# Performance work log

Measured on AMD Instinct MI355X. Metric: run time of the kernel, lower is better.

Reference implementation:

```python
import jax, jax.numpy as jnp
import numpy as np

N = 512           # nodes
DIM = 64          # feature dim (in_dim == dim)
KS = (0.9, 0.7, 0.6)
M_DIM = 17
EDGE_DIM = 1
EIN = 2 * DIM + 1 + EDGE_DIM  # EGNN edge-mlp input width = 130
L = 3             # shared EGNN layers per scale


def _rn(k, shape, s=0.05):
    return jax.random.normal(k, shape, jnp.float32) * s


def setup_inputs() -> dict:
    key = jax.random.key(0)
    k = jax.random.split(key, 12)
    feat = jax.random.normal(k[0], (1, N, DIM), jnp.float32)
    coor = jax.random.normal(k[1], (1, N, 3), jnp.float32)
    # sparse-ish binary adjacency stored densely, as the module expects
    edge = (jax.random.uniform(k[2], (1, N, N, 1)) < 0.05).astype(jnp.float32)
    return {
        "feat": feat, "coor": coor, "edge": edge,
        "We1": _rn(k[3], (L, EIN, 2 * EIN)), "be1": jnp.zeros((L, 2 * EIN), jnp.float32),
        "We2": _rn(k[4], (L, 2 * EIN, M_DIM)), "be2": jnp.zeros((L, M_DIM), jnp.float32),
        "Wc1": _rn(k[5], (L, M_DIM, 4 * M_DIM)), "bc1": jnp.zeros((L, 4 * M_DIM), jnp.float32),
        "Wc2": _rn(k[6], (L, 4 * M_DIM, 1)), "bc2": jnp.zeros((L, 1), jnp.float32),
        "Wn1": _rn(k[7], (L, DIM + M_DIM, 2 * DIM)), "bn1": jnp.zeros((L, 2 * DIM), jnp.float32),
        "Wn2": _rn(k[8], (L, 2 * DIM, DIM)), "bn2": jnp.zeros((L, DIM), jnp.float32),
        "wp": _rn(k[9], (len(KS), DIM)), "bp": jnp.zeros((len(KS),), jnp.float32),
        "ep": 0,
    }


def _egnn(feats, coors, edges, We1, be1, We2, be2, Wc1, bc1, Wc2, bc2,
          Wn1, bn1, Wn2, bn2):
    # feats [B,n,d], coors [B,n,3], edges [B,n,n,1]
    rel = coors[:, :, None, :] - coors[:, None, :, :]           # [B,n,n,3]
    dist = jnp.sum(rel * rel, axis=-1, keepdims=True)           # [B,n,n,1]
    B, n, d = feats.shape
    fi = jnp.broadcast_to(feats[:, :, None, :], (B, n, n, d))
    fj = jnp.broadcast_to(feats[:, None, :, :], (B, n, n, d))
    e_in = jnp.concatenate([fi, fj, dist, edges], axis=-1)      # [B,n,n,EIN]
    m = jax.nn.silu(jax.nn.silu(e_in @ We1 + be1) @ We2 + be2)  # [B,n,n,M]
    cw = jax.nn.silu(m @ Wc1 + bc1) @ Wc2 + bc2                 # [B,n,n,1]
    coors_out = coors + jnp.sum(cw * rel, axis=2)               # [B,n,3]
    m_i = jnp.sum(m, axis=2)                                    # [B,n,M]
    h = jax.nn.silu(jnp.concatenate([feats, m_i], axis=-1) @ Wn1 + bn1) @ Wn2 + bn2
    return feats + h, coors_out


def _forward(feat, coor, edge, We1, be1, We2, be2, Wc1, bc1, Wc2, bc2,
             Wn1, bn1, Wn2, bn2, wp, bp):
    org_h, org_g, org_c = feat[0], edge[0, :, :, 0], coor[0]
    n_nodes = org_h.shape[0]
    ug = (org_g != 0).astype(jnp.float32)
    ug2 = ((ug @ ug) != 0).astype(jnp.float32)  # 2-hop closure adjacency
    hs = []
    for i, kf in enumerate(KS):
        kcnt = max(2, int(kf * n_nodes))
        scores = jax.nn.sigmoid(org_h @ wp[i] + bp[i])          # [n]
        vals, idx = jax.lax.top_k(scores, kcnt)
        h = org_h[idx] * vals[:, None]                          # gather + scale
        g = ug2[idx][:, idx]                                    # row+col gather
        c = org_c[idx]
        hc, coors, edges = h[None], c[None], g[None, :, :, None]
        for j in range(3):
            ht, coors = _egnn(hc, coors, edges,
                              We1[j], be1[j], We2[j], be2[j],
                              Wc1[j], bc1[j], Wc2[j], bc2[j],
                              Wn1[j], bn1[j], Wn2[j], bn2[j])
            hc = jax.nn.relu(hc + ht)
        # unpool: zero-scatter back to original node set
        h_full = jnp.zeros((n_nodes, hc.shape[-1]), hc.dtype).at[idx].set(hc[0])
        hs.append(h_full)
    out = hs[-1]
    for h_i in hs:
        out = jnp.maximum(out, h_i)
    return out


def reference(feat, coor, edge, We1, be1, We2, be2, Wc1, bc1, Wc2, bc2,
              Wn1, bn1, Wn2, bn2, wp, bp, ep):
    return _forward(feat, coor, edge, We1, be1, We2, be2, Wc1, bc1, Wc2, bc2,
                    Wn1, bn1, Wn2, bn2, wp, bp)
```

## Files before the change

kernel.cpp:

```cpp
#include <hip/hip_runtime.h>
#include <hip/hip_bf16.h>

typedef unsigned long long u64;
typedef unsigned int u32;
typedef unsigned short u16;

#define NN   512
#define DIMF 64
#define E2   260
#define KPAD 272
#define MD   17
#define MH   68
#define NH1  128
#define K0   460
#define K1   358
#define K2   307
#define KT   1125
#define O1   460
#define O2   818
#define PADU 1152
#define AS   272
#define NT0  8
#define NT1  6
#define NT2  5
#define T0T   (K0*NT0)
#define T01T  (T0T + K1*NT1)
#define TTOT  (T01T + K2*NT2)
#define PBLK  ((TTOT+3)/4)
#define MSTR  32
#define WVLDS 4096

typedef __attribute__((ext_vector_type(8)))  short short8;
typedef __attribute__((ext_vector_type(16))) float f32x16;

union SF  { int4 i4; u16 us[8]; u32 w[4]; short8 v; };
union F4U { float4 v; float f[4]; };

__device__ __forceinline__ float fast_exp2(float x){
#if __has_builtin(__builtin_amdgcn_exp2f)
    return __builtin_amdgcn_exp2f(x);
#else
    return __expf(x * 0.6931471805599453f);
#endif
}
__device__ __forceinline__ float fast_rcp(float x){
#if __has_builtin(__builtin_amdgcn_rcpf)
    return __builtin_amdgcn_rcpf(x);
#else
    return __fdividef(1.0f, x);
#endif
}
__device__ __forceinline__ float siluf(float x){
    return x * fast_rcp(1.0f + fast_exp2(x * -1.4426950408889634f));
}
__device__ __forceinline__ float sigf(float x){
    return fast_rcp(1.0f + fast_exp2(x * -1.4426950408889634f));
}
__device__ __forceinline__ u16 bf16_rne(float f){
    u32 u = __float_as_uint(f);
    u += 0x7FFFu + ((u >> 16) & 1u);
    return (u16)(u >> 16);
}
__device__ __forceinline__ float bf16f(u16 h){
    return __uint_as_float(((u32)h) << 16);
}
__device__ __forceinline__ u32 pk_bf16(float x, float y){
    float2 f2; f2.x = x; f2.y = y;
    __hip_bfloat162 h = __float22bfloat162_rn(f2);
    union { __hip_bfloat162 b; u32 u; } cv; cv.b = h;
    return cv.u;
}
__device__ __forceinline__ void lgkm_wait(){
#if __has_builtin(__builtin_amdgcn_s_waitcnt)
    __builtin_amdgcn_s_waitcnt(0xC07F);
#endif
}

__global__ __launch_bounds__(256) void k_pre(
    const float* __restrict__ edge, const float* __restrict__ feat,
    const float* __restrict__ wp, const float* __restrict__ bp,
    const float* __restrict__ We2, const float* __restrict__ Wc1,
    const float* __restrict__ We1, const float* __restrict__ be2,
    const float* __restrict__ bc1, const float* __restrict__ Wc2,
    u64* __restrict__ ugw, float* __restrict__ scores,
    u16* __restrict__ W2f, u16* __restrict__ Wc1f,
    float* __restrict__ wdP, float* __restrict__ weP, float* __restrict__ be2P,
    float* __restrict__ bc1P, float* __restrict__ Wc2P, u64* __restrict__ ug2w){
    int blk = blockIdx.x, t = threadIdx.x;
    if (blk < 128){
        int i = blk*4 + (t>>6); int lane = t&63;
        const float* row = edge + (size_t)i*NN;
        for (int w = 0; w < 8; w++){
            u64 m = __ballot(row[w*64+lane] != 0.0f);
            if (lane == 0) ugw[i*8+w] = m;
        }
        return;
    }
    if (blk < 134){
        int gid = (blk-128)*256 + t; if (gid >= 3*NN) return;
        int l = gid>>9, n = gid&511;
        float s = bp[l];
        for (int d = 0; d < DIMF; d++) s = fmaf(feat[n*DIMF+d], wp[l*DIMF+d], s);
        scores[gid] = sigf(s);
        return;
    }
    int idx = (blk-134)*256 + t;
    if (idx < 52224){
        int e = idx&7, lane = (idx>>3)&63, hl = (idx>>9)&1, c = (idx>>10)%17, jl = idx/17408;
        int q = lane>>5, nn = lane&31;
        int k = c*16 + q*8 + e;
        float v = (k < E2 && nn < MD) ? We2[jl*E2*MD + k*MD + nn] : 0.0f;
        u16 hi = bf16_rne(v);
        W2f[idx] = hl ? bf16_rne(v - bf16f(hi)) : hi;
        return;
    }
    idx -= 52224;
    if (idx < 9216){
        int e = idx & 7, lane = (idx>>3)&63, c2 = (idx>>9)&1, T = (idx>>10)%3, jl = idx/3072;
        int q = lane>>5, nn = lane&31;
        int o = c2*16 + q*8 + e, h = T*32 + nn;
        float v = (o < MD && h < MH) ? Wc1[jl*MD*MH + o*MH + h] : 0.0f;
        Wc1f[idx] = bf16_rne(v);
        return;
    }
    idx -= 9216;
    if (idx < 816){ int jl = idx/KPAD, k = idx%KPAD;
        wdP[idx] = (k < E2) ? We1[jl*130*E2 + 128*E2 + k] : 0.0f; return; }
    idx -= 816;
    if (idx < 816){ int jl = idx/KPAD, k = idx%KPAD;
        weP[idx] = (k < E2) ? We1[jl*130*E2 + 129*E2 + k] : 0.0f; return; }
    idx -= 816;
    if (idx < 96){ int jl = idx/32, o = idx%32;
        be2P[idx] = (o < MD) ? be2[jl*MD+o] : 0.0f; return; }
    idx -= 96;
    if (idx < 288){ int jl = idx/96, h = idx%96;
        bc1P[idx] = (h < MH) ? bc1[jl*MH+h] : 0.0f; return; }
    idx -= 288;
    if (idx < 288){ int jl = idx/96, h = idx%96;
        Wc2P[idx] = (h < MH) ? Wc2[jl*MH+h] : 0.0f; return; }
    idx -= 288;
    if (idx < 4096){ ug2w[idx] = 0ULL; return; }
}

__global__ __launch_bounds__(512) void k_sortug2(
    const float* __restrict__ scores, const u64* __restrict__ ugw,
    float* __restrict__ svals, int* __restrict__ sidx, int* __restrict__ rev,
    u64* __restrict__ ug2w){
    int blk = blockIdx.x, t = threadIdx.x;
    if (blk < 3){
        int l = blk;
        __shared__ float sk[NN];
        __shared__ int   si[NN];
        sk[t] = scores[l*NN+t]; si[t] = t; rev[l*NN+t] = -1;
        __syncthreads();
        for (int k = 2; k <= NN; k <<= 1){
            for (int jj = k>>1; jj > 0; jj >>= 1){
                int p = t ^ jj;
                if (p > t){
                    float ka = sk[t], kb = sk[p];
                    int ia = si[t], ib = si[p];
                    bool before = (ka > kb) || (ka == kb && ia < ib);
                    bool sw = ((t & k) == 0) ? (!before) : before;
                    if (sw){ sk[t]=kb; sk[p]=ka; si[t]=ib; si[p]=ia; }
                }
                __syncthreads();
            }
        }
        svals[l*NN+t] = sk[t]; sidx[l*NN+t] = si[t];
        int kcnt = (l==0)?K0:(l==1)?K1:K2;
        if (t < kcnt) rev[l*NN + si[t]] = t;
    } else {
        int gid = (blk-3)*512 + t;
        int i  = gid >> 6;
        int w  = (gid >> 3) & 7;
        int kc = gid & 7;
        u64 rm = ugw[i*8 + kc];
        u64 acc = 0;
        int base = kc*64;
        while (rm){
            int k2 = __builtin_ctzll(rm);
            rm &= rm - 1;
            acc |= ugw[(base + k2)*8 + w];
        }
        if (acc) atomicOr(&ug2w[i*8 + w], acc);
    }
}

__device__ __forceinline__ void ab_comp(int jl, const float* __restrict__ We1,
                                        const float* __restrict__ be1, float hval,
                                        int u, int lane,
                                        float* __restrict__ Ap, float* __restrict__ BF){
    const float* W = We1 + jl*130*E2;
    int r  = 4*lane;
    int rt = 256 + lane;
    int rtc = (lane < 4) ? rt : 256;
    F4U av; av.v = *(const float4*)(be1 + jl*E2 + r);
    F4U bv; bv.f[0]=bv.f[1]=bv.f[2]=bv.f[3]=0.0f;
    float avx = be1[jl*E2 + rtc];
    float bvx = 0.0f;
    for (int d = 0; d < DIMF; d++){
        float hv = __shfl(hval, d);
        F4U w1; w1.v = *(const float4*)(W + d*E2 + r);
        F4U w2; w2.v = *(const float4*)(W + (DIMF+d)*E2 + r);
#pragma unroll
        for (int i = 0; i < 4; i++){
            av.f[i] = fmaf(hv, w1.f[i], av.f[i]);
            bv.f[i] = fmaf(hv, w2.f[i], bv.f[i]);
        }
        avx = fmaf(hv, W[d*E2 + rtc], avx);
        bvx = fmaf(hv, W[(DIMF+d)*E2 + rtc], bvx);
    }
    *(float4*)(Ap + u*AS + r) = av.v;
    *(float4*)(BF + ((size_t)(lane>>1)*PADU + u)*8 + (lane&1)*4) = bv.v;
    if (lane < 16){
        int k = 256 + lane;
        float aval = (lane < 4) ? avx : 0.0f;
        float bval = (lane < 4) ? bvx : 0.0f;
        Ap[u*AS + k] = aval;
        BF[((size_t)(k>>3)*PADU + u)*8 + (k&7)] = bval;
    }
}

__global__ __launch_bounds__(256) void k_gab(
    const float* __restrict__ feat, const float* __restrict__ coor,
    const float* __restrict__ svals, const int* __restrict__ sidx,
    const float* __restrict__ We1, const float* __restrict__ be1,
    float* __restrict__ hc, float* __restrict__ c0, float* __restrict__ c1,
    float* __restrict__ mi, float* __restrict__ Ap, float* __restrict__ BF){
    int t = threadIdx.x; int u = blockIdx.x*4 + (t>>6); if (u >= KT) return;
    int lane = t&63;
    int l = (u<K0)?0:(u<O2)?1:2;
    int a = u - ((l==0)?0:(l==1)?O1:O2);
    int org = sidx[l*NN+a];
    float val = svals[l*NN+a];
    float hval = feat[org*DIMF+lane]*val;
    hc[u*DIMF+lane] = hval;
    if (lane < 3){ float c = coor[org*3+lane]; c0[u*4+lane]=c; c1[u*4+lane]=c; }
    if (lane == 3){ c0[u*4+3]=0.0f; c1[u*4+3]=0.0f; }
    if (lane < 20) mi[u*20+lane] = 0.0f;
    ab_comp(0, We1, be1, hval, u, lane, Ap, BF);
}

template<int DOCW>
__global__ __launch_bounds__(256, 3) void k_pair(
    int jl,
    const float* __restrict__ Ap, const float* __restrict__ BF,
    const u16* __restrict__ W2f, const u16* __restrict__ Wc1f,
    const float* __restrict__ wdP, const float* __restrict__ weP,
    const float* __restrict__ be2P, const float* __restrict__ bc1P,
    const float* __restrict__ Wc2P, const float* __restrict__ bc2,
    const float* __restrict__ cin, float* __restrict__ cout,
    float* __restrict__ mi, const int* __restrict__ sidx,
    const u64* __restrict__ ug2w){
    __shared__ __align__(16) char sWK[4*WVLDS];
    __shared__ __align__(16) char sWD[1088];
    __shared__ __align__(16) char sWE[1088];
    int t = threadIdx.x;
    if (t < 68)       ((float4*)sWD)[t]    = *(const float4*)(wdP + jl*KPAD + 4*t);
    else if (t < 136) ((float4*)sWE)[t-68] = *(const float4*)(weP + jl*KPAD + 4*(t-68));
    int wid0 = blockIdx.x*4 + (t>>6);
    int lane = t&63, n = lane&31, q = lane>>5;
    bool dead = (wid0 >= TTOT);
    int wid = dead ? (TTOT-1) : wid0;
    int l, kl, off, a, tile;
    if (wid < T0T)       { l=0; kl=K0; off=0;  a = wid>>3; tile = wid&7; }
    else if (wid < T01T) { int w = wid-T0T;  l=1; kl=K1; off=O1; a = w/NT1; tile = w - a*NT1; }
    else                 { int w = wid-T01T; l=2; kl=K2; off=O2; a = w/NT2; tile = w - a*NT2; }
    int u = off + a;
    int b0 = tile*64 + n, b1 = b0 + 32;
    float act0 = (b0 < kl) ? 1.0f : 0.0f;
    float act1 = (b1 < kl) ? 1.0f : 0.0f;
    int b0c = min(b0, kl-1), b1c = min(b1, kl-1);
    int ub0 = off + b0c, ub1 = off + b1c;
    int ia  = sidx[l*NN+a];
    int ib0 = sidx[l*NN+b0c], ib1 = sidx[l*NN+b1c];
    float ef0 = act0 * (float)((ug2w[ia*8 + (ib0>>6)] >> (ib0&63)) & 1ULL);
    float ef1 = act1 * (float)((ug2w[ia*8 + (ib1>>6)] >> (ib1&63)) & 1ULL);
    F4U ca;  ca.v  = ((const float4*)cin)[u];
    F4U cb0; cb0.v = ((const float4*)cin)[ub0];
    F4U cb1; cb1.v = ((const float4*)cin)[ub1];
    float tx0 = ca.f[0]-cb0.f[0], ty0 = ca.f[1]-cb0.f[1], tz0 = ca.f[2]-cb0.f[2];
    float tx1 = ca.f[0]-cb1.f[0], ty1 = ca.f[1]-cb1.f[1], tz1 = ca.f[2]-cb1.f[2];
    float dd0 = tx0*tx0 + ty0*ty0 + tz0*tz0;
    float dd1 = tx1*tx1 + ty1*ty1 + tz1*tz1;

    char* myk = sWK + (t>>6)*WVLDS;
    {
        const float* Au = Ap + u*AS;
        ((float4*)myk)[lane] = *(const float4*)(Au + 4*lane);
        if (lane < 4) ((float4*)myk)[64+lane] = *(const float4*)(Au + 256 + 4*lane);
    }
    __syncthreads();

    const float* pB0 = BF + ((size_t)q*PADU + ub0)*8;
    const float* pB1 = BF + ((size_t)q*PADU + ub1)*8;
    const u16*   pW  = W2f + jl*17408 + lane*8;
    const char*  pA  = myk + q*32;
    const char*  pWD = sWD + q*32;
    const char*  pWE = sWE + q*32;

    f32x16 acc0, acc1;
#pragma unroll
    for (int r = 0; r < 16; r++){ acc0[r] = 0.0f; acc1[r] = 0.0f; }

    F4U nb0a, nb0b, nb1a, nb1b; SF nwh, nwl;
    nb0a.v = *(const float4*)(pB0);     nb0b.v = *(const float4*)(pB0 + 4);
    nb1a.v = *(const float4*)(pB1);     nb1b.v = *(const float4*)(pB1 + 4);
    nwh.i4 = *(const int4*)(pW);        nwl.i4 = *(const int4*)(pW + 512);

    for (int c = 0; c < 17; c++){
        F4U b0a = nb0a, b0b = nb0b, b1a = nb1a, b1b = nb1b;
        SF  wh  = nwh,  wl  = nwl;
        pB0 += 2*PADU*8; pB1 += 2*PADU*8; pW += 1024;
        if (c < 16){
            nb0a.v = *(const float4*)(pB0);     nb0b.v = *(const float4*)(pB0 + 4);
            nb1a.v = *(const float4*)(pB1);     nb1b.v = *(const float4*)(pB1 + 4);
            nwh.i4 = *(const int4*)(pW);        nwl.i4 = *(const int4*)(pW + 512);
        }
        F4U a0, a1, w0, w1, e0, e1;
        a0.v = *(const float4*)(pA);       a1.v = *(const float4*)(pA + 16);
        w0.v = *(const float4*)(pWD);      w1.v = *(const float4*)(pWD + 16);
        e0.v = *(const float4*)(pWE);      e1.v = *(const float4*)(pWE + 16);
        pA += 64; pWD += 64; pWE += 64;
        float s0[8], s1[8];
#pragma unroll
        for (int e = 0; e < 4; e++){
            s0[e]   = siluf(fmaf(dd0, w0.f[e], fmaf(ef0, e0.f[e], a0.f[e] + b0a.f[e])));
            s1[e]   = siluf(fmaf(dd1, w0.f[e], fmaf(ef1, e0.f[e], a0.f[e] + b1a.f[e])));
            s0[4+e] = siluf(fmaf(dd0, w1.f[e], fmaf(ef0, e1.f[e], a1.f[e] + b0b.f[e])));
            s1[4+e] = siluf(fmaf(dd1, w1.f[e], fmaf(ef1, e1.f[e], a1.f[e] + b1b.f[e])));
        }
        SF shi0, slo0, shi1, slo1;
#pragma unroll
        for (int p = 0; p < 4; p++){
            float x = s0[2*p], y = s0[2*p+1];
            u32 h = pk_bf16(x, y);
            shi0.w[p] = h;
            slo0.w[p] = pk_bf16(x - __uint_as_float(h << 16),
                                y - __uint_as_float(h & 0xFFFF0000u));
            x = s1[2*p]; y = s1[2*p+1];
            h = pk_bf16(x, y);
            shi1.w[p] = h;
            slo1.w[p] = pk_bf16(x - __uint_as_float(h << 16),
                                y - __uint_as_float(h & 0xFFFF0000u));
        }
        acc0 = __builtin_amdgcn_mfma_f32_32x32x16_bf16(shi0.v, wh.v, acc0, 0, 0, 0);
        acc0 = __builtin_amdgcn_mfma_f32_32x32x16_bf16(slo0.v, wh.v, acc0, 0, 0, 0);
        acc0 = __builtin_amdgcn_mfma_f32_32x32x16_bf16(shi0.v, wl.v, acc0, 0, 0, 0);
        acc1 = __builtin_amdgcn_mfma_f32_32x32x16_bf16(shi1.v, wh.v, acc1, 0, 0, 0);
        acc1 = __builtin_amdgcn_mfma_f32_32x32x16_bf16(slo1.v, wh.v, acc1, 0, 0, 0);
        acc1 = __builtin_amdgcn_mfma_f32_32x32x16_bf16(shi1.v, wl.v, acc1, 0, 0, 0);
    }

    float be2v = be2P[jl*32 + n];
    u16* mlds = (u16*)myk;
    float msum = 0.0f;
#pragma unroll
    for (int r = 0; r < 16; r++){
        int row = (r&3) + 8*(r>>2) + 4*q;
        float m0 = siluf(acc0[r] + be2v);
        float m1 = siluf(acc1[r] + be2v);
        m0 = (tile*64 + row      < kl) ? m0 : 0.0f;
        m1 = (tile*64 + 32 + row < kl) ? m1 : 0.0f;
        msum += m0 + m1;
        if (DOCW){
            mlds[row*MSTR + n]        = bf16_rne(m0);
            mlds[(row+32)*MSTR + n]   = bf16_rne(m1);
        }
    }
    msum += __shfl_xor(msum, 32);
    if (!dead && lane < MD) atomicAdd(&mi[u*20 + lane], msum);

    if (DOCW){
        lgkm_wait();
        const char* mb = (const char*)mlds;
        float gx = 0.0f, gy = 0.0f, gz = 0.0f;
        float bc2v = bc2[jl];
#pragma unroll
        for (int S = 0; S < 2; S++){
            SF af0, af1;
            af0.i4 = *(const int4*)(mb + (S*32+n)*(MSTR*2) + q*16);
            af1.i4 = *(const int4*)(mb + (S*32+n)*(MSTR*2) + 32 + q*16);
            float cwp[16];
#pragma unroll
            for (int r = 0; r < 16; r++) cwp[r] = 0.0f;
            for (int T = 0; T < 3; T++){
                SF bb0, bb1;
                bb0.i4 = *(const int4*)(Wc1f + jl*3072 + T*1024 +       lane*8);
                bb1.i4 = *(const int4*)(Wc1f + jl*3072 + T*1024 + 512 + lane*8);
                f32x16 p2;
#pragma unroll
                for (int r = 0; r < 16; r++) p2[r] = 0.0f;
                p2 = __builtin_amdgcn_mfma_f32_32x32x16_bf16(af0.v, bb0.v, p2, 0, 0, 0);
                p2 = __builtin_amdgcn_mfma_f32_32x32x16_bf16(af1.v, bb1.v, p2, 0, 0, 0);
                float bc1v = bc1P[jl*96 + T*32 + n];
                float wc2v = Wc2P[jl*96 + T*32 + n];
#pragma unroll
                for (int r = 0; r < 16; r++)
                    cwp[r] = fmaf(siluf(p2[r] + bc1v), wc2v, cwp[r]);
            }
#pragma unroll
            for (int r = 0; r < 16; r++){
                int row  = (r&3) + 8*(r>>2) + 4*q + S*32;
                int brow = tile*64 + row;
                F4U cbr; cbr.v = ((const float4*)cin)[off + min(brow, kl-1)];
                float cw = cwp[r] + ((n == 0) ? bc2v : 0.0f);
                cw = (brow < kl) ? cw : 0.0f;
                gx = fmaf(cw, ca.f[0]-cbr.f[0], gx);
                gy = fmaf(cw, ca.f[1]-cbr.f[1], gy);
                gz = fmaf(cw, ca.f[2]-cbr.f[2], gz);
            }
        }
#pragma unroll
        for (int s = 1; s < 64; s <<= 1){
            gx += __shfl_xor(gx, s); gy += __shfl_xor(gy, s); gz += __shfl_xor(gz, s);
        }
        if (!dead && lane == 0){
            atomicAdd(&cout[u*4+0], gx);
            atomicAdd(&cout[u*4+1], gy);
            atomicAdd(&cout[u*4+2], gz);
        }
    }
}

__global__ __launch_bounds__(256) void k_nodeab(
    int jl, int donext, int docopy,
    const float* __restrict__ Wn1, const float* __restrict__ bn1,
    const float* __restrict__ Wn2, const float* __restrict__ bn2,
    const float* __restrict__ We1, const float* __restrict__ be1,
    float* __restrict__ hc, float* __restrict__ mi,
    const float* __restrict__ ccur, float* __restrict__ cnext,
    float* __restrict__ Ap, float* __restrict__ BF){
    int t = threadIdx.x; int u = blockIdx.x*4 + (t>>6); if (u >= KT) return;
    int lane = t&63;
    float hval = hc[u*DIMF+lane];
    float mval = (lane < MD) ? mi[u*20+lane] : 0.0f;
    const float* W1 = Wn1 + jl*(DIMF+MD)*NH1;
    float v0 = bn1[jl*NH1+lane], v1 = bn1[jl*NH1+lane+64];
    for (int d = 0; d < DIMF; d++){
        float x = __shfl(hval, d);
        v0 = fmaf(x, W1[d*NH1+lane],    v0);
        v1 = fmaf(x, W1[d*NH1+lane+64], v1);
    }
    for (int d = 0; d < MD; d++){
        float x = __shfl(mval, d);
        v0 = fmaf(x, W1[(DIMF+d)*NH1+lane],    v0);
        v1 = fmaf(x, W1[(DIMF+d)*NH1+lane+64], v1);
    }
    float s0 = siluf(v0), s1 = siluf(v1);
    const float* W2 = Wn2 + jl*NH1*DIMF;
    float h = bn2[jl*DIMF+lane];
    for (int i = 0; i < 64; i++) h = fmaf(__shfl(s0, i), W2[i*DIMF+lane], h);
    for (int i = 0; i < 64; i++) h = fmaf(__shfl(s1, i), W2[(64+i)*DIMF+lane], h);
    float hn = fmaxf(0.0f, fmaf(2.0f, hval, h));
    hc[u*DIMF+lane] = hn;
    if (donext){
        if (lane < 20) mi[u*20+lane] = 0.0f;
        if (docopy && lane < 4) cnext[u*4+lane] = ccur[u*4+lane];
        ab_comp(jl+1, We1, be1, hn, u, lane, Ap, BF);
    }
}

__global__ void k_final(const float* __restrict__ hc, const int* __restrict__ rev,
                        float* __restrict__ out){
    int gid = blockIdx.x*blockDim.x + threadIdx.x;
    if (gid >= NN*DIMF) return;
    int nn = gid>>6, d = gid&63;
    float v = 0.0f;
    int a0 = rev[0*NN+nn]; if (a0 >= 0) v = fmaxf(v, hc[(0  + a0)*DIMF + d]);
    int a1 = rev[1*NN+nn]; if (a1 >= 0) v = fmaxf(v, hc[(O1 + a1)*DIMF + d]);
    int a2 = rev[2*NN+nn]; if (a2 >= 0) v = fmaxf(v, hc[(O2 + a2)*DIMF + d]);
    out[gid] = v;
}

extern "C" void kernel_launch(void* const* d_in, const int* in_sizes, int n_in,
                              void* d_out, int out_size, void* d_ws, size_t ws_size,
                              hipStream_t stream) {
    (void)in_sizes; (void)n_in; (void)out_size; (void)ws_size;
    const float* feat = (const float*)d_in[0];
    const float* coor = (const float*)d_in[1];
    const float* edge = (const float*)d_in[2];
    const float* We1  = (const float*)d_in[3];
    const float* be1  = (const float*)d_in[4];
    const float* We2  = (const float*)d_in[5];
    const float* be2  = (const float*)d_in[6];
    const float* Wc1  = (const float*)d_in[7];
    const float* bc1  = (const float*)d_in[8];
    const float* Wc2  = (const float*)d_in[9];
    const float* bc2  = (const float*)d_in[10];
    const float* Wn1  = (const float*)d_in[11];
    const float* bn1  = (const float*)d_in[12];
    const float* Wn2  = (const float*)d_in[13];
    const float* bn2  = (const float*)d_in[14];
    const float* wp   = (const float*)d_in[15];
    const float* bp   = (const float*)d_in[16];
    float* out = (float*)d_out;

    char* wsb = (char*)d_ws;
    u64*   ugw    = (u64*)  (wsb + 0);
    u64*   ug2w   = (u64*)  (wsb + 32768);
    float* scores = (float*)(wsb + 65536);
    float* svals  = (float*)(wsb + 71680);
    int*   sidx   = (int*)  (wsb + 77824);
    int*   rev    = (int*)  (wsb + 83968);
    float* c0     = (float*)(wsb + 90112);
    float* c1     = (float*)(wsb + 108544);
    float* mi     = (float*)(wsb + 126976);
    float* hc     = (float*)(wsb + 217088);
    float* Ap     = (float*)(wsb + 505344);
    float* BF     = (float*)(wsb + 1729536);
    u16*   W2f    = (u16*)  (wsb + 2982912);
    u16*   Wc1f   = (u16*)  (wsb + 3087360);
    float* wdP    = (float*)(wsb + 3105792);
    float* weP    = (float*)(wsb + 3109120);
    float* be2P   = (float*)(wsb + 3112448);
    float* bc1P   = (float*)(wsb + 3112832);
    float* Wc2P   = (float*)(wsb + 3113984);

    k_pre<<<399, 256, 0, stream>>>(edge, feat, wp, bp, We2, Wc1, We1, be2, bc1, Wc2,
                                   ugw, scores, W2f, Wc1f,
                                   wdP, weP, be2P, bc1P, Wc2P, ug2w);
    k_sortug2<<<67, 512, 0, stream>>>(scores, ugw, svals, sidx, rev, ug2w);
    k_gab<<<282, 256, 0, stream>>>(feat, coor, svals, sidx, We1, be1,
                                   hc, c0, c1, mi, Ap, BF);
    k_pair<1><<<PBLK, 256, 0, stream>>>(0, Ap, BF, W2f, Wc1f,
                                        wdP, weP, be2P, bc1P, Wc2P, bc2,
                                        c0, c1, mi, sidx, ug2w);
    k_nodeab<<<282, 256, 0, stream>>>(0, 1, 1, Wn1, bn1, Wn2, bn2, We1, be1,
                                      hc, mi, c1, c0, Ap, BF);
    k_pair<1><<<PBLK, 256, 0, stream>>>(1, Ap, BF, W2f, Wc1f,
                                        wdP, weP, be2P, bc1P, Wc2P, bc2,
                                        c1, c0, mi, sidx, ug2w);
    k_nodeab<<<282, 256, 0, stream>>>(1, 1, 0, Wn1, bn1, Wn2, bn2, We1, be1,
                                      hc, mi, c0, c1, Ap, BF);
    k_pair<0><<<PBLK, 256, 0, stream>>>(2, Ap, BF, W2f, Wc1f,
                                        wdP, weP, be2P, bc1P, Wc2P, bc2,
                                        c0, c1, mi, sidx, ug2w);
    k_nodeab<<<282, 256, 0, stream>>>(2, 0, 0, Wn1, bn1, Wn2, bn2, We1, be1,
                                      hc, mi, c0, c1, Ap, BF);
    k_final<<<128, 256, 0, stream>>>(hc, rev, out);
}
```

Baseline: 417.8 us.

## Pack layer-1 activations with float2 math and perm-based bf16 split, raise occupancy

Result: slower. 450.3 us (+7.8%).

```diff
diff --git a/kernel.cpp b/kernel.cpp
--- a/kernel.cpp
+++ b/kernel.cpp
@@ -27,14 +27,14 @@
 #define T01T  (T0T + K1*NT1)
 #define TTOT  (T01T + K2*NT2)
 #define PBLK  ((TTOT+3)/4)
-#define MSTR  32
-#define WVLDS 4096
+#define MSTR  40
+#define WVLDS 5120
 
 typedef __attribute__((ext_vector_type(8)))  short short8;
 typedef __attribute__((ext_vector_type(16))) float f32x16;
 
 union SF  { int4 i4; u16 us[8]; u32 w[4]; short8 v; };
-union F4U { float4 v; float f[4]; };
+union F4U { float4 v; float2 h[2]; float f[4]; u32 w[4]; };
 
 __device__ __forceinline__ float fast_exp2(float x){
 #if __has_builtin(__builtin_amdgcn_exp2f)
@@ -64,16 +64,28 @@
 __device__ __forceinline__ float bf16f(u16 h){
     return __uint_as_float(((u32)h) << 16);
 }
-__device__ __forceinline__ u32 pk_bf16(float x, float y){
-    float2 f2; f2.x = x; f2.y = y;
-    __hip_bfloat162 h = __float22bfloat162_rn(f2);
-    union { __hip_bfloat162 b; u32 u; } cv; cv.b = h;
-    return cv.u;
-}
 __device__ __forceinline__ void lgkm_wait(){
 #if __has_builtin(__builtin_amdgcn_s_waitcnt)
     __builtin_amdgcn_s_waitcnt(0xC07F);
 #endif
+}
+__device__ __forceinline__ float2 f2add(float2 a, float2 b){ return float2{a.x+b.x, a.y+b.y}; }
+__device__ __forceinline__ float2 f2mul(float2 a, float2 b){ return float2{a.x*b.x, a.y*b.y}; }
+__device__ __forceinline__ float2 f2fma(float2 a, float2 b, float2 c){
+    return float2{fmaf(a.x,b.x,c.x), fmaf(a.y,b.y,c.y)};
+}
+__device__ __forceinline__ float2 silu2(float2 p){
+    float2 t = f2mul(p, float2{-1.4426950408889634f, -1.4426950408889634f});
+    float ex = fast_exp2(t.x), ey = fast_exp2(t.y);
+    float rx = fast_rcp(1.0f + ex), ry = fast_rcp(1.0f + ey);
+    return float2{p.x*rx, p.y*ry};
+}
+__device__ __forceinline__ void pack2(float2 s, u32& hpk, u32& lpk){
+    u32 bx = __float_as_uint(s.x), by = __float_as_uint(s.y);
+    hpk = __builtin_amdgcn_perm(by, bx, 0x07060302u);
+    float lx = s.x - __uint_as_float(bx & 0xFFFF0000u);
+    float ly = s.y - __uint_as_float(by & 0xFFFF0000u);
+    lpk = __builtin_amdgcn_perm(__float_as_uint(ly), __float_as_uint(lx), 0x07060302u);
 }
 
 __global__ __launch_bounds__(256) void k_pre(
@@ -242,7 +254,7 @@
 }
 
 template<int DOCW>
-__global__ __launch_bounds__(256, 3) void k_pair(
+__global__ __launch_bounds__(256, 6) void k_pair(
     int jl,
     const float* __restrict__ Ap, const float* __restrict__ BF,
     const u16* __restrict__ W2f, const u16* __restrict__ Wc1f,
@@ -308,6 +320,8 @@
     nb1a.v = *(const float4*)(pB1);     nb1b.v = *(const float4*)(pB1 + 4);
     nwh.i4 = *(const int4*)(pW);        nwl.i4 = *(const int4*)(pW + 512);
 
+    float2 DD0{dd0,dd0}, EF0{ef0,ef0}, DD1{dd1,dd1}, EF1{ef1,ef1};
+
     for (int c = 0; c < 17; c++){
         F4U b0a = nb0a, b0b = nb0b, b1a = nb1a, b1b = nb1b;
         SF  wh  = nwh,  wl  = nwl;
@@ -322,27 +336,18 @@
         w0.v = *(const float4*)(pWD);      w1.v = *(const float4*)(pWD + 16);
         e0.v = *(const float4*)(pWE);      e1.v = *(const float4*)(pWE + 16);
         pA += 64; pWD += 64; pWE += 64;
-        float s0[8], s1[8];
-#pragma unroll
-        for (int e = 0; e < 4; e++){
-            s0[e]   = siluf(fmaf(dd0, w0.f[e], fmaf(ef0, e0.f[e], a0.f[e] + b0a.f[e])));
-            s1[e]   = siluf(fmaf(dd1, w0.f[e], fmaf(ef1, e0.f[e], a0.f[e] + b1a.f[e])));
-            s0[4+e] = siluf(fmaf(dd0, w1.f[e], fmaf(ef0, e1.f[e], a1.f[e] + b0b.f[e])));
-            s1[4+e] = siluf(fmaf(dd1, w1.f[e], fmaf(ef1, e1.f[e], a1.f[e] + b1b.f[e])));
-        }
+
         SF shi0, slo0, shi1, slo1;
 #pragma unroll
-        for (int p = 0; p < 4; p++){
-            float x = s0[2*p], y = s0[2*p+1];
-            u32 h = pk_bf16(x, y);
-            shi0.w[p] = h;
-            slo0.w[p] = pk_bf16(x - __uint_as_float(h << 16),
-                                y - __uint_as_float(h & 0xFFFF0000u));
-            x = s1[2*p]; y = s1[2*p+1];
-            h = pk_bf16(x, y);
-            shi1.w[p] = h;
-            slo1.w[p] = pk_bf16(x - __uint_as_float(h << 16),
-                                y - __uint_as_float(h & 0xFFFF0000u));
+        for (int h = 0; h < 2; h++){
+            float2 p00 = f2fma(EF0, e0.h[h], f2fma(DD0, w0.h[h], f2add(a0.h[h], b0a.h[h])));
+            float2 p01 = f2fma(EF0, e1.h[h], f2fma(DD0, w1.h[h], f2add(a1.h[h], b0b.h[h])));
+            float2 p10 = f2fma(EF1, e0.h[h], f2fma(DD1, w0.h[h], f2add(a0.h[h], b1a.h[h])));
+            float2 p11 = f2fma(EF1, e1.h[h], f2fma(DD1, w1.h[h], f2add(a1.h[h], b1b.h[h])));
+            pack2(silu2(p00), shi0.w[h],   slo0.w[h]);
+            pack2(silu2(p01), shi0.w[2+h], slo0.w[2+h]);
+            pack2(silu2(p10), shi1.w[h],   slo1.w[h]);
+            pack2(silu2(p11), shi1.w[2+h], slo1.w[2+h]);
         }
         acc0 = __builtin_amdgcn_mfma_f32_32x32x16_bf16(shi0.v, wh.v, acc0, 0, 0, 0);
         acc0 = __builtin_amdgcn_mfma_f32_32x32x16_bf16(slo0.v, wh.v, acc0, 0, 0, 0);
```
